# Kernel optimization log

Measured on AMD Instinct MI355X. Metric: run time of the kernel, lower is better.

The kernel has to match this reference:

```python
import jax, jax.numpy as jnp
import numpy as np

D_MODEL, D_STATE, L = 512, 64, 1024
BATCH = 8


def setup_inputs() -> dict:
    key = jax.random.key(0)
    ks = jax.random.split(key, 8)
    dt_min, dt_max = 1e-3, 1e-1
    log_dt = jax.random.uniform(ks[0], (D_MODEL,)) * (np.log(dt_max) - np.log(dt_min)) + np.log(dt_min)
    log_A_real = jnp.log(0.5 * jnp.ones((D_MODEL, D_STATE)))
    A_imag = jnp.pi * jnp.tile(jnp.arange(D_STATE, dtype=jnp.float32), (D_MODEL, 1))
    B_real = jnp.ones((D_MODEL, D_STATE), jnp.float32)
    B_imag = jnp.zeros((D_MODEL, D_STATE), jnp.float32)
    C_real = jax.random.normal(ks[1], (D_MODEL, D_STATE))
    C_imag = jax.random.normal(ks[2], (D_MODEL, D_STATE))
    D = jax.random.normal(ks[3], (D_MODEL,))
    # 1x1 conv (Conv1d kernel_size=1) -> weight (2H, H), bias (2H,)
    conv_w = jax.random.normal(ks[4], (2 * D_MODEL, D_MODEL)) / np.sqrt(D_MODEL)
    conv_b = jnp.zeros((2 * D_MODEL,), jnp.float32)
    dec_w = jax.random.normal(ks[5], (1, D_MODEL)) / np.sqrt(D_MODEL)
    dec_b = jnp.zeros((1,), jnp.float32)
    u = jax.random.normal(ks[6], (BATCH, D_MODEL, L))
    return dict(u=u, log_dt=log_dt, log_A_real=log_A_real, A_imag=A_imag,
                B_real=B_real, B_imag=B_imag, C_real=C_real, C_imag=C_imag,
                D=D, conv_w=conv_w, conv_b=conv_b, dec_w=dec_w, dec_b=dec_b)


def _s4d_kernel(log_dt, log_A_real, A_imag, B_real, B_imag, C_real, C_imag, Lk):
    dt = jnp.exp(log_dt)                              # (H,)
    A = -jnp.exp(log_A_real) + 1j * A_imag            # (H, N) complex
    dtA = A * dt[:, None]                             # (H, N)
    A_bar = jnp.exp(dtA)
    Bc = B_real + 1j * B_imag
    B_bar = (A_bar - 1.0) / A * Bc                    # ZOH discretization
    Cc = C_real + 1j * C_imag
    t = jnp.arange(Lk)                                # (L,)
    # A_bar^t = exp(dtA * t); fuse C*B_bar weighting, reduce over state N
    A_pow = jnp.exp(dtA[:, :, None] * t)              # (H, N, L)
    K = jnp.einsum('hn,hnl->hl', Cc * B_bar, A_pow)   # (H, L) complex
    return K.real


def reference(u, log_dt, log_A_real, A_imag, B_real, B_imag, C_real, C_imag,
              D, conv_w, conv_b, dec_w, dec_b):
    H, Lk = u.shape[1], u.shape[2]
    K = _s4d_kernel(log_dt, log_A_real, A_imag, B_real, B_imag, C_real, C_imag, Lk)
    # depthwise cross-correlation (torch conv1d semantics), padding L-1, keep first L
    y = jax.lax.conv_general_dilated(
        u, K[:, None, :], window_strides=(1,), padding=[(Lk - 1, Lk - 1)],
        feature_group_count=H, dimension_numbers=('NCH', 'OIH', 'NCH'))
    y = y[:, :, :Lk]
    y = y + u * D[:, None]
    y = jax.nn.gelu(y, approximate=False)
    # 1x1 conv + GLU over channel dim
    z = jnp.einsum('oc,bcl->bol', conv_w, y) + conv_b[:, None]
    a, b = jnp.split(z, 2, axis=1)
    y = a * jax.nn.sigmoid(b)                         # (B, H, L)
    pooled = y.mean(axis=-1)                          # (B, H)
    return pooled @ dec_w.T + dec_b                   # (B, 1)
```

## Files before the change

### kernel.cpp

```cpp
#include <hip/hip_runtime.h>
#include <hip/hip_bf16.h>
#include <math.h>

typedef __attribute__((ext_vector_type(8))) short short8;
typedef __attribute__((ext_vector_type(4))) float f32x4;
typedef __attribute__((ext_vector_type(16))) float f32x16;
typedef __attribute__((ext_vector_type(4))) unsigned int uint4v;

constexpr int Hm = 512, Lm = 1024, Bm = 8;

static __device__ __forceinline__ unsigned short f2bf(float f) {
    __hip_bfloat16 h = __float2bfloat16(f);
    return *reinterpret_cast<unsigned short*>(&h);
}
static __device__ __forceinline__ float bf2f(unsigned short u) {
    return __uint_as_float((unsigned)u << 16);
}
static __device__ __forceinline__ uint2 pack4(const unsigned short* x) {
    return make_uint2((unsigned)x[0] | ((unsigned)x[1] << 16),
                      (unsigned)x[2] | ((unsigned)x[3] << 16));
}
static __device__ __forceinline__ short8 ld16u(const char* p) {
    uint2 a = *(const uint2*)p;
    uint2 b = *(const uint2*)(p + 8);
    uint4v t = { a.x, a.y, b.x, b.y };
    return __builtin_bit_cast(short8, t);
}

__global__ __launch_bounds__(256) void k_kgen(const float* __restrict__ log_dt,
                                              const float* __restrict__ log_A_real,
                                              const float* __restrict__ A_imag,
                                              const float* __restrict__ B_real,
                                              const float* __restrict__ B_imag,
                                              const float* __restrict__ C_real,
                                              const float* __restrict__ C_imag,
                                              const float* __restrict__ conv_w,
                                              unsigned int* __restrict__ Krep,
                                              unsigned short* __restrict__ Woh,
                                              unsigned short* __restrict__ Wol) {
    __shared__ __align__(16) char smem[22528];
    const int tid = threadIdx.x, lane = tid & 63, wid = tid >> 6;
    float* kl = (float*)smem + wid * 1056;
    float* Kf = (float*)(smem + 16896);
    float* pl = (float*)(smem + 20992);
    const int h = blockIdx.x;

    {
        int i = h * 1024 + tid * 4;
        float4 v = *(const float4*)&conv_w[i];
        unsigned short h0 = f2bf(v.x), h1 = f2bf(v.y), h2 = f2bf(v.z), h3 = f2bf(v.w);
        unsigned short l0 = f2bf(v.x - bf2f(h0));
        unsigned short l1 = f2bf(v.y - bf2f(h1));
        unsigned short l2 = f2bf(v.z - bf2f(h2));
        unsigned short l3 = f2bf(v.w - bf2f(h3));
        *(uint2*)&Woh[i] = make_uint2((unsigned)h0 | ((unsigned)h1 << 16),
                                      (unsigned)h2 | ((unsigned)h3 << 16));
        *(uint2*)&Wol[i] = make_uint2((unsigned)l0 | ((unsigned)l1 << 16),
                                      (unsigned)l2 | ((unsigned)l3 << 16));
    }
    if (tid < 64) {
        int idx = h * 64 + tid;
        double dt = exp((double)log_dt[h]);
        double Ar = -exp((double)log_A_real[idx]);
        double Ai = (double)A_imag[idx];
        double ar = Ar * dt, ai = Ai * dt;
        double er = exp(ar);
        double rr = er * cos(ai), ri = er * sin(ai);
        double nr = rr - 1.0, ni = ri;
        double den = Ar * Ar + Ai * Ai;
        double qr = (nr * Ar + ni * Ai) / den;
        double qi = (ni * Ar - nr * Ai) / den;
        double Br = (double)B_real[idx], Bi = (double)B_imag[idx];
        double bbr = qr * Br - qi * Bi, bbi = qr * Bi + qi * Br;
        double Cr = (double)C_real[idx], Ci = (double)C_imag[idx];
        double wr = Cr * bbr - Ci * bbi, wi = Cr * bbi + Ci * bbr;
        double e64 = exp(ar * 64.0);
        double p64 = ai * 64.0;
        pl[0 * 64 + tid] = (float)rr;
        pl[1 * 64 + tid] = (float)ri;
        pl[2 * 64 + tid] = (float)wr;
        pl[3 * 64 + tid] = (float)wi;
        pl[4 * 64 + tid] = (float)(e64 * cos(p64));
        pl[5 * 64 + tid] = (float)(e64 * sin(p64));
    }
    __syncthreads();

    const float rrf = pl[0 * 64 + lane], rif = pl[1 * 64 + lane];
    float pr = pl[2 * 64 + lane], pi = pl[3 * 64 + lane];
    float br = pl[4 * 64 + lane], bi = pl[5 * 64 + lane];
    int cc = wid * 4;
    while (cc) {
        if (cc & 1) { float t_ = pr * br - pi * bi; pi = fmaf(pr, bi, pi * br); pr = t_; }
        float t2 = br * br - bi * bi; bi = 2.f * br * bi; br = t2;
        cc >>= 1;
    }
    const int jj = lane & 15, nq = lane >> 4;
    for (int q = 0; q < 16; ++q) {
        #pragma unroll
        for (int j = 0; j < 16; ++j) {
            kl[j * 66 + lane] = pr;
            float t_ = pr * rrf - pi * rif; pi = fmaf(pr, rif, pi * rrf); pr = t_;
        }
        asm volatile("s_waitcnt lgkmcnt(0)" ::: "memory");
        float s0 = 0.f, s1 = 0.f;
        #pragma unroll
        for (int n = 0; n < 16; n += 4) {
            float2 a = *(const float2*)&kl[jj * 66 + nq * 16 + n];
            float2 b2 = *(const float2*)&kl[jj * 66 + nq * 16 + n + 2];
            s0 += a.x + a.y; s1 += b2.x + b2.y;
        }
        float s = s0 + s1;
        s += __shfl_xor(s, 16);
        s += __shfl_xor(s, 32);
        if (lane < 16) Kf[wid * 256 + q * 16 + jj] = s;
        asm volatile("s_waitcnt lgkmcnt(0)" ::: "memory");
    }
    __syncthreads();
    for (int t = tid; t < 2200; t += 256) {
        int s = t / 550;
        int d = t - s * 550;
        int idx0 = 2 * d + s;
        float k0 = (idx0 < 1024) ? Kf[idx0] : 0.f;
        float k1 = (idx0 + 1 < 1024) ? Kf[idx0 + 1] : 0.f;
        Krep[(size_t)h * 2200 + t] = (unsigned)f2bf(k0) | ((unsigned)f2bf(k1) << 16);
    }
}

__global__ __launch_bounds__(256, 2) void k_tconv(const float* __restrict__ u,
                                                  const float* __restrict__ Dvec,
                                                  const unsigned int* __restrict__ Krep,
                                                  unsigned short* __restrict__ YbfH) {
    __shared__ __align__(16) char smem[36160];
    const int tid = threadIdx.x, lane = tid & 63, w = tid >> 6;
    const int h = blockIdx.x;
    const int m = lane & 31, q = lane >> 5;
    const int cg = (lane >> 3) & 3, b = lane & 7;

    {
        const uint4* src = (const uint4*)(Krep + (size_t)h * 2200);
        uint4* dst = (uint4*)smem;
        for (int o = tid; o < 550; o += 256) dst[o] = src[o];
    }
    if (tid < 8) { uint4 z = {0, 0, 0, 0}; ((uint4*)(smem + 36032))[tid] = z; }
    {
        const int b2 = tid >> 5, t32 = tid & 31;
        const float* ub = u + ((size_t)(b2 * 512 + h)) * 1024;
        #pragma unroll
        for (int g = 0; g < 8; ++g) {
            int s = t32 * 4 + g * 128;
            float4 v = *(const float4*)&ub[s];
            unsigned short t0 = f2bf(v.x), t1 = f2bf(v.y), t2 = f2bf(v.z), t3 = f2bf(v.w);
            int jc = s >> 6, e = s & 63;
            *(uint2*)(smem + 17600 + jc * 1152 + b2 * 144 + e * 2) =
                make_uint2((unsigned)t0 | ((unsigned)t1 << 16),
                           (unsigned)t2 | ((unsigned)t3 << 16));
        }
    }
    __syncthreads();

    const int icg = (cg == 0) ? w : (cg == 1) ? 7 - w : (cg == 2) ? 8 + w : 15 - w;
    const int dmax = 15 - w;

    int aU = 17600 + icg * 1152 + b * 144 + q * 16;
    const int zl = 36032 + q * 16;

    const int r = (3 - m) & 3;
    int baseH = r * 2200 + (991 - m - r + 8 * q) * 2;

    const f32x16 zacc = {};
    f32x16 acc0 = zacc, acc1 = zacc;

    short8 m2, m1, w0, w1, w2, w3;
    {
        const char* pH = smem + baseH;
        m2 = ld16u(pH +   0); m1 = ld16u(pH +  32);
        w0 = ld16u(pH +  64); w1 = ld16u(pH +  96);
        w2 = ld16u(pH + 128); w3 = ld16u(pH + 160);
    }

    for (int d = 0; d <= dmax; ++d) {
        const char* pb = smem + ((d <= icg) ? aU : zl);
        short8 b0 = *(const short8*)(pb +  0);
        short8 b1 = *(const short8*)(pb + 32);
        short8 b2 = *(const short8*)(pb + 64);
        short8 b3 = *(const short8*)(pb + 96);
        acc0 = __builtin_amdgcn_mfma_f32_32x32x16_bf16(w0, b0, acc0, 0, 0, 0);
        acc1 = __builtin_amdgcn_mfma_f32_32x32x16_bf16(m2, b0, acc1, 0, 0, 0);
        acc0 = __builtin_amdgcn_mfma_f32_32x32x16_bf16(w1, b1, acc0, 0, 0, 0);
        acc1 = __builtin_amdgcn_mfma_f32_32x32x16_bf16(m1, b1, acc1, 0, 0, 0);
        acc0 = __builtin_amdgcn_mfma_f32_32x32x16_bf16(w2, b2, acc0, 0, 0, 0);
        acc1 = __builtin_amdgcn_mfma_f32_32x32x16_bf16(w0, b2, acc1, 0, 0, 0);
        acc0 = __builtin_amdgcn_mfma_f32_32x32x16_bf16(w3, b3, acc0, 0, 0, 0);
        acc1 = __builtin_amdgcn_mfma_f32_32x32x16_bf16(w1, b3, acc1, 0, 0, 0);
        baseH -= 128; aU -= 1152;
        if (d < dmax) {
            const char* pH = smem + baseH;
            m2 = ld16u(pH +   0); m1 = ld16u(pH +  32);
            w0 = ld16u(pH +  64); w1 = ld16u(pH +  96);
            w2 = ld16u(pH + 128); w3 = ld16u(pH + 160);
        }
    }

    const float Dh = Dvec[h];
    __syncthreads();

    #pragma unroll
    for (int mf = 0; mf < 2; ++mf) {
        const f32x16 ac = mf ? acc1 : acc0;
        #pragma unroll
        for (int rq = 0; rq < 4; ++rq) {
            const int row0 = mf * 32 + 8 * rq + 4 * q;
            uint2 uv2 = *(const uint2*)(smem + 17600 + icg * 1152 + b * 144 + row0 * 2);
            unsigned short us[4] = { (unsigned short)(uv2.x & 0xffff),
                                     (unsigned short)(uv2.x >> 16),
                                     (unsigned short)(uv2.y & 0xffff),
                                     (unsigned short)(uv2.y >> 16) };
            unsigned short oh[4];
            #pragma unroll
            for (int k = 0; k < 4; ++k) {
                float y = ac[rq * 4 + k] + Dh * bf2f(us[k]);
                float g = 0.5f * y * (1.0f + erff(y * 0.70710678118654752f));
                oh[k] = f2bf(g);
            }
            *(uint2*)(smem + icg * 1088 + b * 136 + row0 * 2) = pack4(oh);
        }
    }
    __syncthreads();
    {
        const int b2 = tid >> 5, t32 = tid & 31;
        unsigned short* dst = YbfH + ((size_t)(b2 * 512 + h)) * 1024;
        #pragma unroll
        for (int g = 0; g < 8; ++g) {
            int s = t32 * 4 + g * 128;
            int jc = s >> 6, e = s & 63;
            uint2 v = *(const uint2*)(smem + jc * 1088 + b2 * 136 + e * 2);
            *(uint2*)&dst[s] = v;
        }
    }
}

__global__ __launch_bounds__(256) void k_tr(const unsigned short* __restrict__ Ybf,
                                            unsigned short* __restrict__ Ytb) {
    __shared__ unsigned short tl[64][72];
    const int t = threadIdx.x;
    const int b = blockIdx.z;
    const int c0 = blockIdx.y * 64, l0 = blockIdx.x * 64;
    {
        const int c = t >> 2, lq = (t & 3) * 16;
        const unsigned short* src = Ybf + ((size_t)(b * 512 + c0 + c)) * 1024 + l0 + lq;
        uint4 v0 = *(const uint4*)src;
        uint4 v1 = *(const uint4*)(src + 8);
        *(uint4*)&tl[c][lq] = v0;
        *(uint4*)&tl[c][lq + 8] = v1;
    }
    __syncthreads();
    {
        const int l = t >> 2, cq = (t & 3) * 16;
        unsigned int o[8];
        #pragma unroll
        for (int k = 0; k < 8; ++k)
            o[k] = (unsigned)tl[cq + 2 * k][l] | ((unsigned)tl[cq + 2 * k + 1][l] << 16);
        unsigned short* dst = Ytb + ((size_t)(b * 1024 + l0 + l)) * 512 + c0 + cq;
        *(uint4*)dst = *(uint4*)&o[0];
        *(uint4*)(dst + 8) = *(uint4*)&o[4];
    }
}

__global__ __launch_bounds__(256) void k2_gemm(const unsigned short* __restrict__ WbfH,
                                               const unsigned short* __restrict__ WbfL,
                                               const unsigned short* __restrict__ Ytb,
                                               const float* __restrict__ conv_b,
                                               const float* __restrict__ dec_w,
                                               float* __restrict__ partial) {
    __shared__ unsigned short WTh[128][40], WTl[128][40];
    __shared__ unsigned short YTh[128][40];
    __shared__ float red[4][64][20];
    const int tid = threadIdx.x, lane = tid & 63, wid = tid >> 6;
    const int b = blockIdx.z, oblk = blockIdx.y, lblk = blockIdx.x;
    const int o0 = oblk * 64, l0 = lblk * 128;
    const int fr = lane & 15, fq = lane >> 4;

    f32x4 acc[8][2] = {};

    const int srow = tid >> 1, skh = (tid & 1) * 16;
    const int grow = (srow < 64) ? (o0 + srow) : (512 + o0 + srow - 64);
    const size_t woff = (size_t)grow * 512 + skh;
    const size_t yoff = ((size_t)(b * 1024) + l0 + srow) * 512 + skh;

    for (int c0 = 0; c0 < 512; c0 += 32) {
        __syncthreads();
        uint4 wh0 = *(const uint4*)(WbfH + woff + c0);
        uint4 wh1 = *(const uint4*)(WbfH + woff + c0 + 8);
        uint4 wl0 = *(const uint4*)(WbfL + woff + c0);
        uint4 wl1 = *(const uint4*)(WbfL + woff + c0 + 8);
        uint4 yh0 = *(const uint4*)(Ytb + yoff + c0);
        uint4 yh1 = *(const uint4*)(Ytb + yoff + c0 + 8);
        *(uint4*)&WTh[srow][skh]     = wh0;
        *(uint4*)&WTh[srow][skh + 8] = wh1;
        *(uint4*)&WTl[srow][skh]     = wl0;
        *(uint4*)&WTl[srow][skh + 8] = wl1;
        *(uint4*)&YTh[srow][skh]     = yh0;
        *(uint4*)&YTh[srow][skh + 8] = yh1;
        __syncthreads();
        short8 b0h = *(const short8*)&YTh[wid * 32 + fr][fq * 8];
        short8 b1h = *(const short8*)&YTh[wid * 32 + 16 + fr][fq * 8];
        #pragma unroll
        for (int mf = 0; mf < 8; ++mf) {
            short8 ah = *(const short8*)&WTh[mf * 16 + fr][fq * 8];
            short8 al = *(const short8*)&WTl[mf * 16 + fr][fq * 8];
            acc[mf][0] = __builtin_amdgcn_mfma_f32_16x16x32_bf16(ah, b0h, acc[mf][0], 0, 0, 0);
            acc[mf][1] = __builtin_amdgcn_mfma_f32_16x16x32_bf16(ah, b1h, acc[mf][1], 0, 0, 0);
            acc[mf][0] = __builtin_amdgcn_mfma_f32_16x16x32_bf16(al, b0h, acc[mf][0], 0, 0, 0);
            acc[mf][1] = __builtin_amdgcn_mfma_f32_16x16x32_bf16(al, b1h, acc[mf][1], 0, 0, 0);
        }
    }

    #pragma unroll
    for (int mf = 0; mf < 4; ++mf)
        #pragma unroll
        for (int j = 0; j < 4; ++j) {
            int ol = mf * 16 + fq * 4 + j;
            float ba = conv_b[o0 + ol];
            float bb = conv_b[512 + o0 + ol];
            float s = 0.f;
            #pragma unroll
            for (int nf = 0; nf < 2; ++nf) {
                float za = acc[mf][nf][j] + ba;
                float zb = acc[mf + 4][nf][j] + bb;
                s += za / (1.f + expf(-zb));
            }
            red[wid][ol][fr] = s;
        }
    __syncthreads();
    if (tid < 64) {
        float s = 0.f;
        #pragma unroll
        for (int w = 0; w < 4; ++w) {
            float4 r0 = *(const float4*)&red[w][tid][0];
            float4 r1 = *(const float4*)&red[w][tid][4];
            float4 r2 = *(const float4*)&red[w][tid][8];
            float4 r3 = *(const float4*)&red[w][tid][12];
            s += (r0.x + r0.y + r0.z + r0.w) + (r1.x + r1.y + r1.z + r1.w)
               + (r2.x + r2.y + r2.z + r2.w) + (r3.x + r3.y + r3.z + r3.w);
        }
        float val = s * dec_w[o0 + tid] * (1.0f / 1024.0f);
        #pragma unroll
        for (int off = 32; off; off >>= 1) val += __shfl_xor(val, off);
        if (tid == 0) partial[((b * 8) + oblk) * 8 + lblk] = val;
    }
}

__global__ void k3_final(const float* __restrict__ partial,
                         const float* __restrict__ dec_b,
                         float* __restrict__ out) {
    int b = threadIdx.x;
    if (b < Bm) {
        float s = dec_b[0];
        for (int i = 0; i < 64; ++i) s += partial[b * 64 + i];
        out[b] = s;
    }
}

extern "C" void kernel_launch(void* const* d_in, const int* in_sizes, int n_in,
                              void* d_out, int out_size, void* d_ws, size_t ws_size,
                              hipStream_t stream) {
    const float* u          = (const float*)d_in[0];
    const float* log_dt     = (const float*)d_in[1];
    const float* log_A_real = (const float*)d_in[2];
    const float* A_imag     = (const float*)d_in[3];
    const float* B_real     = (const float*)d_in[4];
    const float* B_imag     = (const float*)d_in[5];
    const float* C_real     = (const float*)d_in[6];
    const float* C_imag     = (const float*)d_in[7];
    const float* Dvec       = (const float*)d_in[8];
    const float* conv_w     = (const float*)d_in[9];
    const float* conv_b     = (const float*)d_in[10];
    const float* dec_w      = (const float*)d_in[11];
    const float* dec_b      = (const float*)d_in[12];

    char* base = (char*)d_ws;
    unsigned int* Krep   = (unsigned int*)base;
    unsigned short* YbfH = (unsigned short*)(base + 4718592);
    unsigned short* Ytb  = (unsigned short*)(base + 13107200);
    unsigned short* Wh   = (unsigned short*)(base + 21495808);
    unsigned short* Wl   = (unsigned short*)(base + 22544384);
    float* partial       = (float*)(base + 23592960);
    float* out           = (float*)d_out;

    k_kgen<<<512, 256, 0, stream>>>(log_dt, log_A_real, A_imag, B_real, B_imag,
                                    C_real, C_imag, conv_w, Krep, Wh, Wl);
    k_tconv<<<512, 256, 0, stream>>>(u, Dvec, Krep, YbfH);
    k_tr<<<dim3(16, 8, 8), 256, 0, stream>>>(YbfH, Ytb);
    k2_gemm<<<dim3(8, 8, 8), 256, 0, stream>>>(Wh, Wl, Ytb, conv_b, dec_w, partial);
    k3_final<<<1, 64, 0, stream>>>(partial, dec_b, out);
}
```

Baseline: 67.66 us.

## Drop bf16 low-part weight split and fuse transpose into GEMM tile load

Removes the separate transpose kernel by having the GEMM read the channel-major bf16 activations directly, interleaving pairs of channel rows in registers and writing a transposed tile into padded shared memory. It also drops the low-order bf16 residual of the weights, halving the MFMA count and the weight traffic. This removes one launch plus a full round trip of the intermediate tensor, but lowers the precision of the 1x1 conv weights to plain bf16, which may affect accuracy.

```diff
diff --git a/kernel.cpp b/kernel.cpp
--- a/kernel.cpp
+++ b/kernel.cpp
@@ -36,8 +36,7 @@
                                               const float* __restrict__ C_imag,
                                               const float* __restrict__ conv_w,
                                               unsigned int* __restrict__ Krep,
-                                              unsigned short* __restrict__ Woh,
-                                              unsigned short* __restrict__ Wol) {
+                                              unsigned short* __restrict__ Woh) {
     __shared__ __align__(16) char smem[22528];
     const int tid = threadIdx.x, lane = tid & 63, wid = tid >> 6;
     float* kl = (float*)smem + wid * 1056;
@@ -48,15 +47,8 @@
     {
         int i = h * 1024 + tid * 4;
         float4 v = *(const float4*)&conv_w[i];
-        unsigned short h0 = f2bf(v.x), h1 = f2bf(v.y), h2 = f2bf(v.z), h3 = f2bf(v.w);
-        unsigned short l0 = f2bf(v.x - bf2f(h0));
-        unsigned short l1 = f2bf(v.y - bf2f(h1));
-        unsigned short l2 = f2bf(v.z - bf2f(h2));
-        unsigned short l3 = f2bf(v.w - bf2f(h3));
-        *(uint2*)&Woh[i] = make_uint2((unsigned)h0 | ((unsigned)h1 << 16),
-                                      (unsigned)h2 | ((unsigned)h3 << 16));
-        *(uint2*)&Wol[i] = make_uint2((unsigned)l0 | ((unsigned)l1 << 16),
-                                      (unsigned)l2 | ((unsigned)l3 << 16));
+        *(uint2*)&Woh[i] = make_uint2((unsigned)f2bf(v.x) | ((unsigned)f2bf(v.y) << 16),
+                                      (unsigned)f2bf(v.z) | ((unsigned)f2bf(v.w) << 16));
     }
     if (tid < 64) {
         int idx = h * 64 + tid;
@@ -239,41 +231,13 @@
     }
 }
 
-__global__ __launch_bounds__(256) void k_tr(const unsigned short* __restrict__ Ybf,
-                                            unsigned short* __restrict__ Ytb) {
-    __shared__ unsigned short tl[64][72];
-    const int t = threadIdx.x;
-    const int b = blockIdx.z;
-    const int c0 = blockIdx.y * 64, l0 = blockIdx.x * 64;
-    {
-        const int c = t >> 2, lq = (t & 3) * 16;
-        const unsigned short* src = Ybf + ((size_t)(b * 512 + c0 + c)) * 1024 + l0 + lq;
-        uint4 v0 = *(const uint4*)src;
-        uint4 v1 = *(const uint4*)(src + 8);
-        *(uint4*)&tl[c][lq] = v0;
-        *(uint4*)&tl[c][lq + 8] = v1;
-    }
-    __syncthreads();
-    {
-        const int l = t >> 2, cq = (t & 3) * 16;
-        unsigned int o[8];
-        #pragma unroll
-        for (int k = 0; k < 8; ++k)
-            o[k] = (unsigned)tl[cq + 2 * k][l] | ((unsigned)tl[cq + 2 * k + 1][l] << 16);
-        unsigned short* dst = Ytb + ((size_t)(b * 1024 + l0 + l)) * 512 + c0 + cq;
-        *(uint4*)dst = *(uint4*)&o[0];
-        *(uint4*)(dst + 8) = *(uint4*)&o[4];
-    }
-}
-
 __global__ __launch_bounds__(256) void k2_gemm(const unsigned short* __restrict__ WbfH,
-                                               const unsigned short* __restrict__ WbfL,
-                                               const unsigned short* __restrict__ Ytb,
+                                               const unsigned short* __restrict__ Ybf,
                                                const float* __restrict__ conv_b,
                                                const float* __restrict__ dec_w,
                                                float* __restrict__ partial) {
-    __shared__ unsigned short WTh[128][40], WTl[128][40];
-    __shared__ unsigned short YTh[128][40];
+    __shared__ unsigned short WTh[128][40];
+    __shared__ unsigned short YT[128][44];
     __shared__ float red[4][64][20];
     const int tid = threadIdx.x, lane = tid & 63, wid = tid >> 6;
     const int b = blockIdx.z, oblk = blockIdx.y, lblk = blockIdx.x;
@@ -285,33 +249,36 @@
     const int srow = tid >> 1, skh = (tid & 1) * 16;
     const int grow = (srow < 64) ? (o0 + srow) : (512 + o0 + srow - 64);
     const size_t woff = (size_t)grow * 512 + skh;
-    const size_t yoff = ((size_t)(b * 1024) + l0 + srow) * 512 + skh;
+    const int cp = tid & 15, lg = tid >> 4;
 
     for (int c0 = 0; c0 < 512; c0 += 32) {
         __syncthreads();
         uint4 wh0 = *(const uint4*)(WbfH + woff + c0);
         uint4 wh1 = *(const uint4*)(WbfH + woff + c0 + 8);
-        uint4 wl0 = *(const uint4*)(WbfL + woff + c0);
-        uint4 wl1 = *(const uint4*)(WbfL + woff + c0 + 8);
-        uint4 yh0 = *(const uint4*)(Ytb + yoff + c0);
-        uint4 yh1 = *(const uint4*)(Ytb + yoff + c0 + 8);
+        const unsigned short* ys0 = Ybf + ((size_t)(b * 512 + c0 + 2 * cp)) * 1024 + l0 + lg * 8;
+        uint4 y0 = *(const uint4*)ys0;
+        uint4 y1 = *(const uint4*)(ys0 + 1024);
         *(uint4*)&WTh[srow][skh]     = wh0;
         *(uint4*)&WTh[srow][skh + 8] = wh1;
-        *(uint4*)&WTl[srow][skh]     = wl0;
-        *(uint4*)&WTl[srow][skh + 8] = wl1;
-        *(uint4*)&YTh[srow][skh]     = yh0;
-        *(uint4*)&YTh[srow][skh + 8] = yh1;
+        {
+            const unsigned int* a = (const unsigned int*)&y0;
+            const unsigned int* c = (const unsigned int*)&y1;
+            #pragma unroll
+            for (int t2 = 0; t2 < 4; ++t2) {
+                unsigned int lo = (a[t2] & 0xffffu) | (c[t2] << 16);
+                unsigned int hi = (a[t2] >> 16) | (c[t2] & 0xffff0000u);
+                *(unsigned int*)&YT[lg * 8 + 2 * t2][2 * cp] = lo;
+                *(unsigned int*)&YT[lg * 8 + 2 * t2 + 1][2 * cp] = hi;
+            }
+        }
         __syncthreads();
-        short8 b0h = *(const short8*)&YTh[wid * 32 + fr][fq * 8];
-        short8 b1h = *(const short8*)&YTh[wid * 32 + 16 + fr][fq * 8];
+        short8 b0h = ld16u((const char*)&YT[wid * 32 + fr][fq * 8]);
+        short8 b1h = ld16u((const char*)&YT[wid * 32 + 16 + fr][fq * 8]);
         #pragma unroll
         for (int mf = 0; mf < 8; ++mf) {
             short8 ah = *(const short8*)&WTh[mf * 16 + fr][fq * 8];
-            short8 al = *(const short8*)&WTl[mf * 16 + fr][fq * 8];
             acc[mf][0] = __builtin_amdgcn_mfma_f32_16x16x32_bf16(ah, b0h, acc[mf][0], 0, 0, 0);
             acc[mf][1] = __builtin_amdgcn_mfma_f32_16x16x32_bf16(ah, b1h, acc[mf][1], 0, 0, 0);
-            acc[mf][0] = __builtin_amdgcn_mfma_f32_16x16x32_bf16(al, b0h, acc[mf][0], 0, 0, 0);
-            acc[mf][1] = __builtin_amdgcn_mfma_f32_16x16x32_bf16(al, b1h, acc[mf][1], 0, 0, 0);
         }
     }
 
@@ -381,16 +348,13 @@
     char* base = (char*)d_ws;
     unsigned int* Krep   = (unsigned int*)base;
     unsigned short* YbfH = (unsigned short*)(base + 4718592);
-    unsigned short* Ytb  = (unsigned short*)(base + 13107200);
-    unsigned short* Wh   = (unsigned short*)(base + 21495808);
-    unsigned short* Wl   = (unsigned short*)(base + 22544384);
-    float* partial       = (float*)(base + 23592960);
+    unsigned short* Wh   = (unsigned short*)(base + 13107200);
+    float* partial       = (float*)(base + 14155776);
     float* out           = (float*)d_out;
 
     k_kgen<<<512, 256, 0, stream>>>(log_dt, log_A_real, A_imag, B_real, B_imag,
-                                    C_real, C_imag, conv_w, Krep, Wh, Wl);
+                                    C_real, C_imag, conv_w, Krep, Wh);
     k_tconv<<<512, 256, 0, stream>>>(u, Dvec, Krep, YbfH);
-    k_tr<<<dim3(16, 8, 8), 256, 0, stream>>>(YbfH, Ytb);
-    k2_gemm<<<dim3(8, 8, 8), 256, 0, stream>>>(Wh, Wl, Ytb, conv_b, dec_w, partial);
+    k2_gemm<<<dim3(8, 8, 8), 256, 0, stream>>>(Wh, YbfH, conv_b, dec_w, partial);
     k3_final<<<1, 64, 0, stream>>>(partial, dec_b, out);
 }
```

Result: faster. 61.53 us (-9.1%).
